# Kernel optimization log

Hardware: AMD Instinct MI355X
Metric: run time of the kernel (lower is better)

Reference implementation:

```python
import jax, jax.numpy as jnp
import numpy as np

EMBED = 1024
HEADS = 16
HEAD_DIM = EMBED // HEADS  # 64 quantum wires


def setup_inputs() -> dict:
    key = jax.random.key(0)
    ks = jax.random.split(key, 6)
    s = 1.0 / np.sqrt(EMBED)
    return {
        "x": jax.random.normal(ks[0], (8, 4096, EMBED), dtype=jnp.float32),
        "Wk": jax.random.normal(ks[1], (EMBED, EMBED), dtype=jnp.float32) * s,
        "Wq": jax.random.normal(ks[2], (EMBED, EMBED), dtype=jnp.float32) * s,
        "Wv": jax.random.normal(ks[3], (EMBED, EMBED), dtype=jnp.float32) * s,
        "Wo": jax.random.normal(ks[4], (EMBED, EMBED), dtype=jnp.float32) * s,
        "theta": jax.random.normal(ks[5], (HEAD_DIM,), dtype=jnp.float32),
    }


def reference(x, Wk, Wq, Wv, Wo, theta):
    b, s, _ = x.shape
    # linear projections (torch Linear: y = x @ W^T), split heads -> [b,s,h,d]
    def proj(W):
        return (x @ W.T).reshape(b, s, HEADS, HEAD_DIM)
    k, q, v = proj(Wk), proj(Wq), proj(Wv)
    # QLayer: per-wire RX(x_i) then trainable RX(theta_i) on |0>, measure PauliZ
    # -> <Z_i> = cos(x_i + theta_i) exactly (product state, independent wires).
    k_q = jnp.cos(k + theta)
    q_q = jnp.cos(q + theta)
    v_q = jnp.cos(v + theta)
    # Faithful to source: matmul over last two dims of [b,s,h,d] -> attention
    # across the HEADS axis ([b,s,h,h]), not across sequence.
    scores = jnp.einsum('bsid,bsjd->bsij', q_q, k_q) / jnp.sqrt(
        jnp.asarray(HEAD_DIM, dtype=x.dtype))
    attn = jax.nn.softmax(scores, axis=-1)  # dropout = identity at inference
    out = jnp.einsum('bsij,bsjd->bsid', attn, v_q).reshape(b, s, EMBED)
    return out @ Wo.T
```

## Files before the change

### kernel.cpp

```cpp
#include <hip/hip_runtime.h>
#include <hip/hip_fp16.h>

#define NTOK 32768
#define NE   1024

typedef _Float16 half_t;
typedef _Float16 f16x8 __attribute__((ext_vector_type(8)));
typedef _Float16 f16x4 __attribute__((ext_vector_type(4)));
typedef float    f32x4 __attribute__((ext_vector_type(4)));

typedef __attribute__((address_space(1))) const unsigned int guint;
typedef __attribute__((address_space(3))) unsigned int luint;

__device__ __forceinline__ void async16(const void* g, void* l) {
    __builtin_amdgcn_global_load_lds((guint*)g, (luint*)l, 16, 0, 0);
}

__global__ __launch_bounds__(256) void cvt_f32_f16(const float* __restrict__ s,
                                                   half_t* __restrict__ d, int n) {
    int i = (blockIdx.x * 256 + threadIdx.x) * 8;
    if (i >= n) return;
    float4 a = *(const float4*)(s + i);
    float4 b = *(const float4*)(s + i + 4);
    f16x8 h = {(_Float16)a.x, (_Float16)a.y, (_Float16)a.z, (_Float16)a.w,
               (_Float16)b.x, (_Float16)b.y, (_Float16)b.z, (_Float16)b.w};
    *(f16x8*)(d + i) = h;
}


#define WAITV(N) asm volatile("s_waitcnt vmcnt(" #N ")" ::: "memory")
#define BARRIER()                              \
    do {                                       \
        asm volatile("" ::: "memory");         \
        __builtin_amdgcn_s_barrier();          \
        asm volatile("" ::: "memory");         \
    } while (0)

#define ASC(b, c) (Asm + ((b) * 2 + (c)) * 8192)
#define BSC(b, c) (Bsm + ((b) * 2 + (c)) * 8192)

#define STAGE_A(dst, q, k0)                                                   \
    do {                                                                      \
        _Pragma("unroll") for (int l = 0; l < 2; ++l)                         \
            async16(Ag + (size_t)(l * 128 + (q) * 64 + rr) * K + (k0) + cc,   \
                    (char*)(dst) + l * 8192 + w * 1024);                      \
    } while (0)

#define STAGE_B(dst, r, k0)                                                   \
    do {                                                                      \
        _Pragma("unroll") for (int l = 0; l < 2; ++l)                         \
            async16(Bg + (size_t)((l * 2 + wb) * 64 + (r) * 32 + (rr & 31)) * K + \
                        (k0) + cc,                                            \
                    (char*)(dst) + l * 8192 + w * 1024);                      \
    } while (0)

#define READ_A(dstf, b, q)                                                    \
    do {                                                                      \
        _Pragma("unroll") for (int i = 0; i < 4; ++i)                         \
        _Pragma("unroll") for (int x = 0; x < 2; ++x)                         \
            dstf[i][x] = *(const f16x8*)&ASC(b, q)[(wr * 64 + i * 16 + l16) * 64 + \
                                                   (((x * 4 + quad) ^ sw) * 8)]; \
    } while (0)

#define READ_B(dstf, b, r)                                                    \
    do {                                                                      \
        _Pragma("unroll") for (int i2 = 0; i2 < 2; ++i2)                      \
        _Pragma("unroll") for (int x = 0; x < 2; ++x)                         \
            dstf[i2][x] = *(const f16x8*)&BSC(b, r)[(wc * 32 + i2 * 16 + l16) * 64 + \
                                                    (((x * 4 + quad) ^ sw) * 8)]; \
    } while (0)

#define MMA(af, bf, QA, RB)                                                   \
    do {                                                                      \
        __builtin_amdgcn_s_setprio(1);                                        \
        _Pragma("unroll") for (int i = 0; i < 4; ++i)                         \
        _Pragma("unroll") for (int jj = 0; jj < 2; ++jj)                      \
        _Pragma("unroll") for (int x = 0; x < 2; ++x)                         \
            acc[(QA) * 4 + i][(RB) * 2 + jj] =                                \
                __builtin_amdgcn_mfma_f32_16x16x32_f16(                       \
                    af[i][x], bf[jj][x], acc[(QA) * 4 + i][(RB) * 2 + jj], 0, 0, 0); \
        __builtin_amdgcn_s_setprio(0);                                        \
    } while (0)

template <bool QKV>
__global__ __launch_bounds__(512, 2) void gemm_bt(const half_t* __restrict__ A,
                                                  const half_t* __restrict__ Bbase,
                                                  void* __restrict__ Cout,
                                                  const float* __restrict__ theta) {
    constexpr int K  = 1024;
    constexpr int NT = 16;
    constexpr int J  = QKV ? 12 : 4;
    __shared__ alignas(16) half_t smem[65536];
    half_t* Asm = smem;
    half_t* Bsm = smem + 32768;

    const int id    = blockIdx.x;
    const int xcd   = id & 7;
    const int slot  = id >> 3;
    const int ygrp  = slot / J;
    const int j     = slot - ygrp * J;
    const int mtile = ygrp * 8 + xcd;
    const int zsl   = QKV ? (j >> 2) : 0;
    const int xt    = QKV ? (j & 3) : j;

    const int tid  = threadIdx.x;
    const int w    = tid >> 6;
    const int lane = tid & 63;
    const int quad = lane >> 4;
    const int l16  = lane & 15;
    const int sw   = l16 & 7;
    const int wr   = w >> 2, wc = w & 3;
    const size_t m0 = (size_t)mtile * 256;
    const int    n0 = xt * 256;

    const half_t* Ag = A + m0 * K;
    const half_t* Bg = Bbase + (size_t)zsl * (size_t)(NE * NE) + (size_t)n0 * K;

    const int rr = tid >> 3;
    const int cc = ((tid & 7) ^ (rr & 7)) * 8;
    const int wb = tid >> 8;

    f32x4 acc[8][4];
#pragma unroll
    for (int i = 0; i < 8; ++i)
#pragma unroll
        for (int jj = 0; jj < 4; ++jj) acc[i][jj] = (f32x4){0.f, 0.f, 0.f, 0.f};

    STAGE_A(ASC(0, 0), 0, 0);
    STAGE_B(BSC(0, 0), 0, 0);
    STAGE_B(BSC(0, 1), 1, 0);
    STAGE_A(ASC(0, 1), 1, 0);
    STAGE_A(ASC(1, 0), 0, 64);
    STAGE_B(BSC(1, 0), 0, 64);
    STAGE_B(BSC(1, 1), 1, 64);
    STAGE_A(ASC(1, 1), 1, 64);
    WAITV(12);
    BARRIER();

    f16x8 aF0[4][2], aF1[4][2], bF0[2][2], bF1[2][2];
    READ_A(aF0, 0, 0);
    READ_B(bF0, 0, 0);
    BARRIER();

    for (int t = 0; t < NT - 2; ++t) {
        const int cur = t & 1, nxt = cur ^ 1;
        const int kf = (t + 2) * 64;
        STAGE_A(ASC(cur, 0), 0, kf);
        MMA(aF0, bF0, 0, 0);
        WAITV(12);
        BARRIER();
        READ_B(bF1, cur, 1);
        STAGE_B(BSC(cur, 0), 0, kf);
        MMA(aF0, bF1, 0, 1);
        WAITV(12);
        BARRIER();
        READ_A(aF1, cur, 1);
        STAGE_B(BSC(cur, 1), 1, kf);
        MMA(aF1, bF1, 1, 1);
        BARRIER();
        STAGE_A(ASC(cur, 1), 1, kf);
        MMA(aF1, bF0, 1, 0);
        WAITV(12);
        BARRIER();
        READ_A(aF0, nxt, 0);
        READ_B(bF0, nxt, 0);
        BARRIER();
    }
    {
        MMA(aF0, bF0, 0, 0);
        WAITV(10);
        BARRIER();
        READ_B(bF1, 0, 1);
        MMA(aF0, bF1, 0, 1);
        WAITV(8);
        BARRIER();
        READ_A(aF1, 0, 1);
        MMA(aF1, bF1, 1, 1);
        MMA(aF1, bF0, 1, 0);
        WAITV(4);
        BARRIER();
        READ_A(aF0, 1, 0);
        READ_B(bF0, 1, 0);
    }
    {
        MMA(aF0, bF0, 0, 0);
        WAITV(2);
        BARRIER();
        READ_B(bF1, 1, 1);
        MMA(aF0, bF1, 0, 1);
        WAITV(0);
        BARRIER();
        READ_A(aF1, 1, 1);
        MMA(aF1, bF1, 1, 1);
        MMA(aF1, bF0, 1, 0);
    }
    __syncthreads();

    if (QKV) {
        half_t* Cl = smem;
#pragma unroll
        for (int nt = 0; nt < 4; ++nt) {
            const int col = wc * 64 + nt * 16 + l16;
            const float th = theta[col & 63];
#pragma unroll
            for (int mt = 0; mt < 8; ++mt) {
                const int rowb = wr * 128 + mt * 16 + quad * 4;
#pragma unroll
                for (int r = 0; r < 4; ++r) {
                    const int row = rowb + r;
                    Cl[row * 256 + (col ^ (((row >> 2) & 3) << 4))] =
                        (half_t)__cosf(acc[mt][nt][r] + th);
                }
            }
        }
        __syncthreads();
        half_t* Cg = (half_t*)Cout + (size_t)zsl * ((size_t)NTOK * NE);
#pragma unroll
        for (int it = 0; it < 16; ++it) {
            const int row = it * 16 + (tid >> 5);
            const int seg = tid & 31;
            f16x8 vv = *(const f16x8*)&Cl[row * 256 +
                                          ((seg * 8) ^ (((row >> 2) & 3) << 4))];
            *(f16x8*)&Cg[(m0 + row) * NE + n0 + seg * 8] = vv;
        }
    } else {
        float* ClF = (float*)smem;
        float* Cg  = (float*)Cout;
#pragma unroll
        for (int s = 0; s < 2; ++s) {
            if (wr == s) {
#pragma unroll
                for (int nt = 0; nt < 4; ++nt) {
                    const int col = wc * 64 + nt * 16 + l16;
#pragma unroll
                    for (int mt = 0; mt < 8; ++mt) {
                        const int rowb = mt * 16 + quad * 4;
#pragma unroll
                        for (int r = 0; r < 4; ++r) {
                            const int row = rowb + r;
                            ClF[row * 256 + (col ^ (((row >> 2) & 1) << 4))] =
                                acc[mt][nt][r];
                        }
                    }
                }
            }
            __syncthreads();
#pragma unroll
            for (int it = 0; it < 16; ++it) {
                const int row = it * 8 + (tid >> 6);
                const int seg = tid & 63;
                f32x4 vv = *(const f32x4*)&ClF[row * 256 +
                                               ((seg * 4) ^ (((row >> 2) & 1) << 4))];
                *(f32x4*)&Cg[(m0 + s * 128 + row) * NE + n0 + seg * 4] = vv;
            }
            __syncthreads();
        }
    }
}

__global__ __launch_bounds__(256) void attn_kernel(const half_t* __restrict__ q,
                                                   const half_t* __restrict__ k,
                                                   const half_t* __restrict__ v,
                                                   half_t* __restrict__ out) {
    __shared__ half_t vT[4][64][20];
    __shared__ half_t Pl[4][16][20];
    const int tid  = threadIdx.x;
    const int w    = tid >> 6;
    const int lane = tid & 63;
    const int quad = lane >> 4;
    const int l16  = lane & 15;
    const size_t base = ((size_t)blockIdx.x * 4 + w) * 1024;

    {
        const int h = lane >> 2, d0 = (lane & 3) * 16;
        f16x8 va = *(const f16x8*)(v + base + h * 64 + d0);
        f16x8 vb = *(const f16x8*)(v + base + h * 64 + d0 + 8);
#pragma unroll
        for (int z = 0; z < 8; ++z) {
            vT[w][d0 + z][h]     = va[z];
            vT[w][d0 + 8 + z][h] = vb[z];
        }
    }

    f16x8 aq0 = *(const f16x8*)(q + base + l16 * 64 + quad * 8);
    f16x8 aq1 = *(const f16x8*)(q + base + l16 * 64 + 32 + quad * 8);
    f16x8 bk0 = *(const f16x8*)(k + base + l16 * 64 + quad * 8);
    f16x8 bk1 = *(const f16x8*)(k + base + l16 * 64 + 32 + quad * 8);
    f32x4 S = __builtin_amdgcn_mfma_f32_16x16x32_f16(aq0, bk0, (f32x4){0.f,0.f,0.f,0.f}, 0, 0, 0);
    S = __builtin_amdgcn_mfma_f32_16x16x32_f16(aq1, bk1, S, 0, 0, 0);

#pragma unroll
    for (int r = 0; r < 4; ++r) {
        float s = S[r] * 0.125f;
        float mx = s;
#pragma unroll
        for (int o = 8; o; o >>= 1) mx = fmaxf(mx, __shfl_xor(mx, o));
        float e = __expf(s - mx);
        float sum = e;
#pragma unroll
        for (int o = 8; o; o >>= 1) sum += __shfl_xor(sum, o);
        Pl[w][quad * 4 + r][l16] = (half_t)(e / sum);
    }
    __syncthreads();

    f16x4 ap = *(const f16x4*)&Pl[w][l16][quad * 4];
#pragma unroll
    for (int c = 0; c < 4; ++c) {
        f16x4 bv = *(const f16x4*)&vT[w][c * 16 + l16][quad * 4];
        f32x4 O = __builtin_amdgcn_mfma_f32_16x16x16f16(ap, bv, (f32x4){0.f,0.f,0.f,0.f}, 0, 0, 0);
#pragma unroll
        for (int r = 0; r < 4; ++r)
            out[base + (quad * 4 + r) * 64 + c * 16 + l16] = (half_t)O[r];
    }
}

extern "C" void kernel_launch(void* const* d_in, const int* in_sizes, int n_in,
                              void* d_out, int out_size, void* d_ws, size_t ws_size,
                              hipStream_t stream) {
    const float* x     = (const float*)d_in[0];
    const float* Wk    = (const float*)d_in[1];
    const float* Wq    = (const float*)d_in[2];
    const float* Wv    = (const float*)d_in[3];
    const float* Wo    = (const float*)d_in[4];
    const float* theta = (const float*)d_in[5];

    char* ws = (char*)d_ws;
    half_t* xh  = (half_t*)ws;
    half_t* wh  = (half_t*)(ws + (size_t)(64 << 20));
    half_t* qkv = (half_t*)(ws + (size_t)(72 << 20));

    cvt_f32_f16<<<NTOK * NE / 2048, 256, 0, stream>>>(x, xh, NTOK * NE);
    cvt_f32_f16<<<NE * NE / 2048, 256, 0, stream>>>(Wq, wh + 0 * NE * NE, NE * NE);
    cvt_f32_f16<<<NE * NE / 2048, 256, 0, stream>>>(Wk, wh + 1 * NE * NE, NE * NE);
    cvt_f32_f16<<<NE * NE / 2048, 256, 0, stream>>>(Wv, wh + 2 * NE * NE, NE * NE);
    cvt_f32_f16<<<NE * NE / 2048, 256, 0, stream>>>(Wo, wh + 3 * NE * NE, NE * NE);

    gemm_bt<true><<<1536, 512, 0, stream>>>(xh, wh, qkv, theta);

    attn_kernel<<<NTOK / 4, 256, 0, stream>>>(qkv, qkv + (size_t)NTOK * NE,
                                              qkv + 2 * (size_t)NTOK * NE, xh);

    gemm_bt<false><<<512, 512, 0, stream>>>(xh, wh + 3 * NE * NE, d_out, nullptr);
}
```

Measured before the change: 568.7 us.

## Load GEMM B operand directly from global into registers, merge weight conversions

The GEMM no longer stages the weight (B) tiles through LDS. Each wave loads its B fragments straight from global memory into registers a k-step ahead, and only A goes through the async LDS double buffer, which cuts the number of barriers per iteration. The four weight fp32-to-fp16 conversion launches are merged into a single 2D-grid kernel. The trade-off is that B is now read uncoalesced from global/L2 with less reuse across waves, and registers carry all fragments.

```diff
diff --git a/kernel.cpp b/kernel.cpp
--- a/kernel.cpp
+++ b/kernel.cpp
@@ -27,30 +27,36 @@
     *(f16x8*)(d + i) = h;
 }
 
+__global__ __launch_bounds__(256) void cvt4_f32_f16(const float* __restrict__ s0,
+                                                    const float* __restrict__ s1,
+                                                    const float* __restrict__ s2,
+                                                    const float* __restrict__ s3,
+                                                    half_t* __restrict__ d) {
+    const float* srcs[4] = {s0, s1, s2, s3};
+    const float* s = srcs[blockIdx.y];
+    int i = (blockIdx.x * 256 + threadIdx.x) * 8;
+    float4 a = *(const float4*)(s + i);
+    float4 b = *(const float4*)(s + i + 4);
+    f16x8 h = {(_Float16)a.x, (_Float16)a.y, (_Float16)a.z, (_Float16)a.w,
+               (_Float16)b.x, (_Float16)b.y, (_Float16)b.z, (_Float16)b.w};
+    *(f16x8*)(d + (size_t)blockIdx.y * (NE * NE) + i) = h;
+}
+
 
 #define WAITV(N) asm volatile("s_waitcnt vmcnt(" #N ")" ::: "memory")
-#define BARRIER()                              \
-    do {                                       \
-        asm volatile("" ::: "memory");         \
-        __builtin_amdgcn_s_barrier();          \
-        asm volatile("" ::: "memory");         \
+#define SYNC()                                             \
+    do {                                                   \
+        asm volatile("s_waitcnt lgkmcnt(0)" ::: "memory"); \
+        __builtin_amdgcn_s_barrier();                      \
+        asm volatile("" ::: "memory");                     \
     } while (0)
 
 #define ASC(b, c) (Asm + ((b) * 2 + (c)) * 8192)
-#define BSC(b, c) (Bsm + ((b) * 2 + (c)) * 8192)
 
 #define STAGE_A(dst, q, k0)                                                   \
     do {                                                                      \
         _Pragma("unroll") for (int l = 0; l < 2; ++l)                         \
             async16(Ag + (size_t)(l * 128 + (q) * 64 + rr) * K + (k0) + cc,   \
-                    (char*)(dst) + l * 8192 + w * 1024);                      \
-    } while (0)
-
-#define STAGE_B(dst, r, k0)                                                   \
-    do {                                                                      \
-        _Pragma("unroll") for (int l = 0; l < 2; ++l)                         \
-            async16(Bg + (size_t)((l * 2 + wb) * 64 + (r) * 32 + (rr & 31)) * K + \
-                        (k0) + cc,                                            \
                     (char*)(dst) + l * 8192 + w * 1024);                      \
     } while (0)
 
@@ -62,12 +68,12 @@
                                                    (((x * 4 + quad) ^ sw) * 8)]; \
     } while (0)
 
-#define READ_B(dstf, b, r)                                                    \
+#define LOADB(dst, RB, kt)                                                    \
     do {                                                                      \
-        _Pragma("unroll") for (int i2 = 0; i2 < 2; ++i2)                      \
+        _Pragma("unroll") for (int jj = 0; jj < 2; ++jj)                      \
         _Pragma("unroll") for (int x = 0; x < 2; ++x)                         \
-            dstf[i2][x] = *(const f16x8*)&BSC(b, r)[(wc * 32 + i2 * 16 + l16) * 64 + \
-                                                    (((x * 4 + quad) ^ sw) * 8)]; \
+            dst[jj][x] = *(const f16x8*)(Bq +                                 \
+                (size_t)((RB) * 32 + jj * 16) * K + (kt) * 64 + x * 32);      \
     } while (0)
 
 #define MMA(af, bf, QA, RB)                                                   \
@@ -92,7 +98,6 @@
     constexpr int J  = QKV ? 12 : 4;
     __shared__ alignas(16) half_t smem[65536];
     half_t* Asm = smem;
-    half_t* Bsm = smem + 32768;
 
     const int id    = blockIdx.x;
     const int xcd   = id & 7;
@@ -115,10 +120,10 @@
 
     const half_t* Ag = A + m0 * K;
     const half_t* Bg = Bbase + (size_t)zsl * (size_t)(NE * NE) + (size_t)n0 * K;
+    const half_t* Bq = Bg + (size_t)(wc * 64 + l16) * K + quad * 8;
 
     const int rr = tid >> 3;
     const int cc = ((tid & 7) ^ (rr & 7)) * 8;
-    const int wb = tid >> 8;
 
     f32x4 acc[8][4];
 #pragma unroll
@@ -126,73 +131,54 @@
 #pragma unroll
         for (int jj = 0; jj < 4; ++jj) acc[i][jj] = (f32x4){0.f, 0.f, 0.f, 0.f};
 
+    f16x8 aF0[4][2], aF1[4][2], bB0[2][2], bB1[2][2];
+
     STAGE_A(ASC(0, 0), 0, 0);
-    STAGE_B(BSC(0, 0), 0, 0);
-    STAGE_B(BSC(0, 1), 1, 0);
     STAGE_A(ASC(0, 1), 1, 0);
     STAGE_A(ASC(1, 0), 0, 64);
-    STAGE_B(BSC(1, 0), 0, 64);
-    STAGE_B(BSC(1, 1), 1, 64);
+    LOADB(bB0, 0, 0);
     STAGE_A(ASC(1, 1), 1, 64);
-    WAITV(12);
-    BARRIER();
-
-    f16x8 aF0[4][2], aF1[4][2], bF0[2][2], bF1[2][2];
+    WAITV(8);
+    SYNC();
     READ_A(aF0, 0, 0);
-    READ_B(bF0, 0, 0);
-    BARRIER();
-
-    for (int t = 0; t < NT - 2; ++t) {
+    READ_A(aF1, 0, 1);
+
+    for (int t = 0; t <= NT - 3; ++t) {
         const int cur = t & 1, nxt = cur ^ 1;
         const int kf = (t + 2) * 64;
+        LOADB(bB1, 1, t);
+        MMA(aF0, bB0, 0, 0);
+        SYNC();
         STAGE_A(ASC(cur, 0), 0, kf);
-        MMA(aF0, bF0, 0, 0);
-        WAITV(12);
-        BARRIER();
-        READ_B(bF1, cur, 1);
-        STAGE_B(BSC(cur, 0), 0, kf);
-        MMA(aF0, bF1, 0, 1);
-        WAITV(12);
-        BARRIER();
-        READ_A(aF1, cur, 1);
-        STAGE_B(BSC(cur, 1), 1, kf);
-        MMA(aF1, bF1, 1, 1);
-        BARRIER();
+        MMA(aF1, bB0, 1, 0);
+        LOADB(bB0, 0, t + 1);
+        MMA(aF1, bB1, 1, 1);
+        MMA(aF0, bB1, 0, 1);
+        WAITV(10);
+        SYNC();
+        READ_A(aF0, nxt, 0);
+        READ_A(aF1, nxt, 1);
         STAGE_A(ASC(cur, 1), 1, kf);
-        MMA(aF1, bF0, 1, 0);
-        WAITV(12);
-        BARRIER();
-        READ_A(aF0, nxt, 0);
-        READ_B(bF0, nxt, 0);
-        BARRIER();
     }
     {
-        MMA(aF0, bF0, 0, 0);
-        WAITV(10);
-        BARRIER();
-        READ_B(bF1, 0, 1);
-        MMA(aF0, bF1, 0, 1);
+        LOADB(bB1, 1, NT - 2);
+        MMA(aF0, bB0, 0, 0);
+        SYNC();
+        MMA(aF1, bB0, 1, 0);
+        LOADB(bB0, 0, NT - 1);
+        MMA(aF1, bB1, 1, 1);
+        MMA(aF0, bB1, 0, 1);
         WAITV(8);
-        BARRIER();
-        READ_A(aF1, 0, 1);
-        MMA(aF1, bF1, 1, 1);
-        MMA(aF1, bF0, 1, 0);
-        WAITV(4);
-        BARRIER();
+        SYNC();
         READ_A(aF0, 1, 0);
-        READ_B(bF0, 1, 0);
+        READ_A(aF1, 1, 1);
     }
     {
-        MMA(aF0, bF0, 0, 0);
-        WAITV(2);
-        BARRIER();
-        READ_B(bF1, 1, 1);
-        MMA(aF0, bF1, 0, 1);
-        WAITV(0);
-        BARRIER();
-        READ_A(aF1, 1, 1);
-        MMA(aF1, bF1, 1, 1);
-        MMA(aF1, bF0, 1, 0);
+        LOADB(bB1, 1, NT - 1);
+        MMA(aF0, bB0, 0, 0);
+        MMA(aF1, bB0, 1, 0);
+        MMA(aF1, bB1, 1, 1);
+        MMA(aF0, bB1, 0, 1);
     }
     __syncthreads();
 
@@ -330,10 +316,7 @@
     half_t* qkv = (half_t*)(ws + (size_t)(72 << 20));
 
     cvt_f32_f16<<<NTOK * NE / 2048, 256, 0, stream>>>(x, xh, NTOK * NE);
-    cvt_f32_f16<<<NE * NE / 2048, 256, 0, stream>>>(Wq, wh + 0 * NE * NE, NE * NE);
-    cvt_f32_f16<<<NE * NE / 2048, 256, 0, stream>>>(Wk, wh + 1 * NE * NE, NE * NE);
-    cvt_f32_f16<<<NE * NE / 2048, 256, 0, stream>>>(Wv, wh + 2 * NE * NE, NE * NE);
-    cvt_f32_f16<<<NE * NE / 2048, 256, 0, stream>>>(Wo, wh + 3 * NE * NE, NE * NE);
+    cvt4_f32_f16<<<dim3(NE * NE / 2048, 4), 256, 0, stream>>>(Wq, Wk, Wv, Wo, wh);
 
     gemm_bt<true><<<1536, 512, 0, stream>>>(xh, wh, qkv, theta);
 
```

After: 675.4 us. +18.8%, slower.

## Make GEMM persistent with next-tile prefetch overlapping epilogue, merge weight conversions

Applied to the files above, without the earlier changes.

Turns the GEMM kernel into a persistent kernel with 256 blocks. Each block loops over several output tiles and prefetches the first K-slices of the next tile during the tail of the current one. The epilogue now stages its output through the free halves of the shared-memory buffers, so it no longer clobbers prefetched data. The four weight-conversion launches are merged into one 2D launch. The aim is to hide per-tile prologue and epilogue latency and cut launch overhead, at the cost of more complex wait-count bookkeeping and a possible tail imbalance with fewer blocks.

```diff
diff --git a/kernel.cpp b/kernel.cpp
--- a/kernel.cpp
+++ b/kernel.cpp
@@ -27,29 +27,50 @@
     *(f16x8*)(d + i) = h;
 }
 
+__global__ __launch_bounds__(256) void cvt4_f32_f16(const float* __restrict__ s0,
+                                                    const float* __restrict__ s1,
+                                                    const float* __restrict__ s2,
+                                                    const float* __restrict__ s3,
+                                                    half_t* __restrict__ d) {
+    const float* srcs[4] = {s0, s1, s2, s3};
+    const float* s = srcs[blockIdx.y];
+    int i = (blockIdx.x * 256 + threadIdx.x) * 8;
+    float4 a = *(const float4*)(s + i);
+    float4 b = *(const float4*)(s + i + 4);
+    f16x8 h = {(_Float16)a.x, (_Float16)a.y, (_Float16)a.z, (_Float16)a.w,
+               (_Float16)b.x, (_Float16)b.y, (_Float16)b.z, (_Float16)b.w};
+    *(f16x8*)(d + (size_t)blockIdx.y * (NE * NE) + i) = h;
+}
+
 
 #define WAITV(N) asm volatile("s_waitcnt vmcnt(" #N ")" ::: "memory")
-#define BARRIER()                              \
+#define BAR()                                  \
     do {                                       \
         asm volatile("" ::: "memory");         \
         __builtin_amdgcn_s_barrier();          \
         asm volatile("" ::: "memory");         \
     } while (0)
+#define BARL()                                             \
+    do {                                                   \
+        asm volatile("s_waitcnt lgkmcnt(0)" ::: "memory"); \
+        __builtin_amdgcn_s_barrier();                      \
+        asm volatile("" ::: "memory");                     \
+    } while (0)
 
 #define ASC(b, c) (Asm + ((b) * 2 + (c)) * 8192)
 #define BSC(b, c) (Bsm + ((b) * 2 + (c)) * 8192)
 
-#define STAGE_A(dst, q, k0)                                                   \
+#define STAGE_A(P, dst, q, k0)                                                \
     do {                                                                      \
         _Pragma("unroll") for (int l = 0; l < 2; ++l)                         \
-            async16(Ag + (size_t)(l * 128 + (q) * 64 + rr) * K + (k0) + cc,   \
+            async16((P) + (size_t)(l * 128 + (q) * 64 + rr) * K + (k0) + cc,  \
                     (char*)(dst) + l * 8192 + w * 1024);                      \
     } while (0)
 
-#define STAGE_B(dst, r, k0)                                                   \
+#define STAGE_B(P, dst, r, k0)                                                \
     do {                                                                      \
         _Pragma("unroll") for (int l = 0; l < 2; ++l)                         \
-            async16(Bg + (size_t)((l * 2 + wb) * 64 + (r) * 32 + (rr & 31)) * K + \
+            async16((P) + (size_t)((l * 2 + wb) * 64 + (r) * 32 + (rr & 31)) * K + \
                         (k0) + cc,                                            \
                     (char*)(dst) + l * 8192 + w * 1024);                      \
     } while (0)
@@ -87,21 +108,15 @@
                                                   const half_t* __restrict__ Bbase,
                                                   void* __restrict__ Cout,
                                                   const float* __restrict__ theta) {
-    constexpr int K  = 1024;
-    constexpr int NT = 16;
-    constexpr int J  = QKV ? 12 : 4;
+    constexpr int K     = 1024;
+    constexpr int J     = QKV ? 12 : 4;
+    constexpr int ITERS = QKV ? 6 : 2;
     __shared__ alignas(16) half_t smem[65536];
     half_t* Asm = smem;
     half_t* Bsm = smem + 32768;
 
-    const int id    = blockIdx.x;
-    const int xcd   = id & 7;
-    const int slot  = id >> 3;
-    const int ygrp  = slot / J;
-    const int j     = slot - ygrp * J;
-    const int mtile = ygrp * 8 + xcd;
-    const int zsl   = QKV ? (j >> 2) : 0;
-    const int xt    = QKV ? (j & 3) : j;
+    const int id  = blockIdx.x;
+    const int xcd = id & 7;
 
     const int tid  = threadIdx.x;
     const int w    = tid >> 6;
@@ -110,150 +125,210 @@
     const int l16  = lane & 15;
     const int sw   = l16 & 7;
     const int wr   = w >> 2, wc = w & 3;
-    const size_t m0 = (size_t)mtile * 256;
-    const int    n0 = xt * 256;
-
-    const half_t* Ag = A + m0 * K;
-    const half_t* Bg = Bbase + (size_t)zsl * (size_t)(NE * NE) + (size_t)n0 * K;
 
     const int rr = tid >> 3;
     const int cc = ((tid & 7) ^ (rr & 7)) * 8;
     const int wb = tid >> 8;
 
+    auto decode = [&](int v, const half_t*& Agp, const half_t*& Bgp,
+                      size_t& m0o, int& n0o, int& zso) {
+        const int slot = v >> 3;
+        const int yg   = slot / J;
+        const int jx   = slot - yg * J;
+        const int mt   = yg * 8 + xcd;
+        zso = QKV ? (jx >> 2) : 0;
+        const int xtt = QKV ? (jx & 3) : jx;
+        m0o = (size_t)mt * 256;
+        n0o = xtt * 256;
+        Agp = A + m0o * K;
+        Bgp = Bbase + (size_t)zso * (size_t)(NE * NE) + (size_t)n0o * K;
+    };
+
+    f16x8 aF0[4][2], aF1[4][2], bF0[2][2], bF1[2][2];
     f32x4 acc[8][4];
-#pragma unroll
-    for (int i = 0; i < 8; ++i)
-#pragma unroll
-        for (int jj = 0; jj < 4; ++jj) acc[i][jj] = (f32x4){0.f, 0.f, 0.f, 0.f};
-
-    STAGE_A(ASC(0, 0), 0, 0);
-    STAGE_B(BSC(0, 0), 0, 0);
-    STAGE_B(BSC(0, 1), 1, 0);
-    STAGE_A(ASC(0, 1), 1, 0);
-    STAGE_A(ASC(1, 0), 0, 64);
-    STAGE_B(BSC(1, 0), 0, 64);
-    STAGE_B(BSC(1, 1), 1, 64);
-    STAGE_A(ASC(1, 1), 1, 64);
-    WAITV(12);
-    BARRIER();
-
-    f16x8 aF0[4][2], aF1[4][2], bF0[2][2], bF1[2][2];
-    READ_A(aF0, 0, 0);
-    READ_B(bF0, 0, 0);
-    BARRIER();
-
-    for (int t = 0; t < NT - 2; ++t) {
-        const int cur = t & 1, nxt = cur ^ 1;
-        const int kf = (t + 2) * 64;
-        STAGE_A(ASC(cur, 0), 0, kf);
-        MMA(aF0, bF0, 0, 0);
-        WAITV(12);
-        BARRIER();
-        READ_B(bF1, cur, 1);
-        STAGE_B(BSC(cur, 0), 0, kf);
-        MMA(aF0, bF1, 0, 1);
-        WAITV(12);
-        BARRIER();
-        READ_A(aF1, cur, 1);
-        STAGE_B(BSC(cur, 1), 1, kf);
-        MMA(aF1, bF1, 1, 1);
-        BARRIER();
-        STAGE_A(ASC(cur, 1), 1, kf);
-        MMA(aF1, bF0, 1, 0);
-        WAITV(12);
-        BARRIER();
-        READ_A(aF0, nxt, 0);
-        READ_B(bF0, nxt, 0);
-        BARRIER();
-    }
-    {
-        MMA(aF0, bF0, 0, 0);
-        WAITV(10);
-        BARRIER();
-        READ_B(bF1, 0, 1);
-        MMA(aF0, bF1, 0, 1);
+
+    for (int it = 0; it < ITERS; ++it) {
+        const bool more = (it + 1 < ITERS);
+        const half_t *Ag, *Bg, *Agn = nullptr, *Bgn = nullptr;
+        size_t m0, m0n;
+        int n0, zsl, n0n, zn;
+        decode(id + it * 256, Ag, Bg, m0, n0, zsl);
+        if (more) decode(id + (it + 1) * 256, Agn, Bgn, m0n, n0n, zn);
+
+#pragma unroll
+        for (int i = 0; i < 8; ++i)
+#pragma unroll
+            for (int jj = 0; jj < 4; ++jj) acc[i][jj] = (f32x4){0.f, 0.f, 0.f, 0.f};
+
+        if (it == 0) {
+            STAGE_B(Bg, BSC(0, 0), 0, 0);
+            STAGE_A(Ag, ASC(0, 0), 0, 0);
+            STAGE_B(Bg, BSC(0, 1), 1, 0);
+            STAGE_A(Ag, ASC(0, 1), 1, 0);
+        }
+        STAGE_B(Bg, BSC(1, 0), 0, 64);
+        STAGE_A(Ag, ASC(1, 0), 0, 64);
+        STAGE_B(Bg, BSC(1, 1), 1, 64);
+        STAGE_A(Ag, ASC(1, 1), 1, 64);
         WAITV(8);
-        BARRIER();
-        READ_A(aF1, 0, 1);
-        MMA(aF1, bF1, 1, 1);
-        MMA(aF1, bF0, 1, 0);
-        WAITV(4);
-        BARRIER();
-        READ_A(aF0, 1, 0);
-        READ_B(bF0, 1, 0);
-    }
-    {
-        MMA(aF0, bF0, 0, 0);
-        WAITV(2);
-        BARRIER();
-        READ_B(bF1, 1, 1);
-        MMA(aF0, bF1, 0, 1);
-        WAITV(0);
-        BARRIER();
-        READ_A(aF1, 1, 1);
-        MMA(aF1, bF1, 1, 1);
-        MMA(aF1, bF0, 1, 0);
-    }
-    __syncthreads();
-
-    if (QKV) {
-        half_t* Cl = smem;
-#pragma unroll
-        for (int nt = 0; nt < 4; ++nt) {
-            const int col = wc * 64 + nt * 16 + l16;
-            const float th = theta[col & 63];
-#pragma unroll
-            for (int mt = 0; mt < 8; ++mt) {
-                const int rowb = wr * 128 + mt * 16 + quad * 4;
-#pragma unroll
-                for (int r = 0; r < 4; ++r) {
-                    const int row = rowb + r;
-                    Cl[row * 256 + (col ^ (((row >> 2) & 3) << 4))] =
-                        (half_t)__cosf(acc[mt][nt][r] + th);
-                }
-            }
+        BAR();
+        READ_A(aF0, 0, 0);
+        READ_B(bF0, 0, 0);
+        BAR();
+
+        for (int t = 0; t < 14; ++t) {
+            const int cur = t & 1, nxt = cur ^ 1;
+            const int kf = (t + 2) * 64;
+            STAGE_B(Bg, BSC(cur, 0), 0, kf);
+            MMA(aF0, bF0, 0, 0);
+            WAITV(12);
+            BAR();
+            READ_B(bF1, cur, 1);
+            STAGE_A(Ag, ASC(cur, 0), 0, kf);
+            MMA(aF0, bF1, 0, 1);
+            WAITV(12);
+            BAR();
+            READ_A(aF1, cur, 1);
+            STAGE_B(Bg, BSC(cur, 1), 1, kf);
+            MMA(aF1, bF1, 1, 1);
+            MMA(aF1, bF0, 1, 0);
+            WAITV(10);
+            BAR();
+            READ_A(aF0, nxt, 0);
+            READ_B(bF0, nxt, 0);
+            STAGE_A(Ag, ASC(cur, 1), 1, kf);
+            BAR();
         }
-        __syncthreads();
-        half_t* Cg = (half_t*)Cout + (size_t)zsl * ((size_t)NTOK * NE);
-#pragma unroll
-        for (int it = 0; it < 16; ++it) {
-            const int row = it * 16 + (tid >> 5);
-            const int seg = tid & 31;
-            f16x8 vv = *(const f16x8*)&Cl[row * 256 +
-                                          ((seg * 8) ^ (((row >> 2) & 3) << 4))];
-            *(f16x8*)&Cg[(m0 + row) * NE + n0 + seg * 8] = vv;
+        if (more) {
+            STAGE_B(Bgn, BSC(0, 0), 0, 0);
+            MMA(aF0, bF0, 0, 0);
+            WAITV(12);
+            BAR();
+            READ_B(bF1, 0, 1);
+            STAGE_A(Agn, ASC(0, 0), 0, 0);
+            MMA(aF0, bF1, 0, 1);
+            WAITV(12);
+            BAR();
+            READ_A(aF1, 0, 1);
+            STAGE_B(Bgn, BSC(0, 1), 1, 0);
+            MMA(aF1, bF1, 1, 1);
+            MMA(aF1, bF0, 1, 0);
+            WAITV(10);
+            BAR();
+            READ_A(aF0, 1, 0);
+            READ_B(bF0, 1, 0);
+            STAGE_A(Agn, ASC(0, 1), 1, 0);
+            BAR();
+            MMA(aF0, bF0, 0, 0);
+            WAITV(10);
+            BAR();
+            READ_B(bF1, 1, 1);
+            MMA(aF0, bF1, 0, 1);
+            WAITV(8);
+            BAR();
+            READ_A(aF1, 1, 1);
+            MMA(aF1, bF1, 1, 1);
+            MMA(aF1, bF0, 1, 0);
+        } else {
+            MMA(aF0, bF0, 0, 0);
+            WAITV(10);
+            BAR();
+            READ_B(bF1, 0, 1);
+            MMA(aF0, bF1, 0, 1);
+            WAITV(8);
+            BAR();
+            READ_A(aF1, 0, 1);
+            MMA(aF1, bF1, 1, 1);
+            MMA(aF1, bF0, 1, 0);
+            WAITV(4);
+            BAR();
+            READ_A(aF0, 1, 0);
+            READ_B(bF0, 1, 0);
+            MMA(aF0, bF0, 0, 0);
+            WAITV(2);
+            BAR();
+            READ_B(bF1, 1, 1);
+            MMA(aF0, bF1, 0, 1);
+            WAITV(0);
+            BAR();
+            READ_A(aF1, 1, 1);
+            MMA(aF1, bF1, 1, 1);
+            MMA(aF1, bF0, 1, 0);
         }
-    } else {
-        float* ClF = (float*)smem;
-        float* Cg  = (float*)Cout;
-#pragma unroll
-        for (int s = 0; s < 2; ++s) {
-            if (wr == s) {
-#pragma unroll
-                for (int nt = 0; nt < 4; ++nt) {
-                    const int col = wc * 64 + nt * 16 + l16;
-#pragma unroll
-                    for (int mt = 0; mt < 8; ++mt) {
-                        const int rowb = mt * 16 + quad * 4;
-#pragma unroll
-                        for (int r = 0; r < 4; ++r) {
-                            const int row = rowb + r;
-                            ClF[row * 256 + (col ^ (((row >> 2) & 1) << 4))] =
-                                acc[mt][nt][r];
+
+        BARL();
+        half_t* Ep0 = Asm + 16384;
+        half_t* Ep1 = Bsm + 16384;
+
+        if (QKV) {
+            half_t* Cg = (half_t*)Cout + (size_t)zsl * ((size_t)NTOK * NE);
+#pragma unroll
+            for (int s = 0; s < 2; ++s) {
+                if (wr == s) {
+#pragma unroll
+                    for (int nt = 0; nt < 4; ++nt) {
+                        const int col = wc * 64 + nt * 16 + l16;
+                        const float th = theta[col & 63];
+#pragma unroll
+                        for (int mt = 0; mt < 8; ++mt) {
+#pragma unroll
+                            for (int r4 = 0; r4 < 4; ++r4) {
+                                const int r = mt * 16 + quad * 4 + r4;
+                                half_t* piece = (r < 64) ? Ep0 : Ep1;
+                                piece[(r & 63) * 256 +
+                                      (col ^ (((r >> 2) & 3) << 4))] =
+                                    (half_t)__cosf(acc[mt][nt][r4] + th);
+                            }
                         }
                     }
                 }
+                BARL();
+#pragma unroll
+                for (int itx = 0; itx < 8; ++itx) {
+                    const int row = itx * 16 + (tid >> 5);
+                    const int seg = tid & 31;
+                    const half_t* piece = (row < 64) ? Ep0 : Ep1;
+                    f16x8 vv = *(const f16x8*)&piece[(row & 63) * 256 +
+                                                     ((seg * 8) ^ (((row >> 2) & 3) << 4))];
+                    *(f16x8*)&Cg[(m0 + s * 128 + row) * NE + n0 + seg * 8] = vv;
+                }
+                BARL();
             }
-            __syncthreads();
-#pragma unroll
-            for (int it = 0; it < 16; ++it) {
-                const int row = it * 8 + (tid >> 6);
-                const int seg = tid & 63;
-                f32x4 vv = *(const f32x4*)&ClF[row * 256 +
-                                               ((seg * 4) ^ (((row >> 2) & 1) << 4))];
-                *(f32x4*)&Cg[(m0 + s * 128 + row) * NE + n0 + seg * 4] = vv;
+        } else {
+            float* Cg  = (float*)Cout;
+            float* Fp0 = (float*)Ep0;
+            float* Fp1 = (float*)Ep1;
+#pragma unroll
+            for (int s = 0; s < 4; ++s) {
+                if (wr == (s >> 1)) {
+#pragma unroll
+                    for (int nt = 0; nt < 4; ++nt) {
+                        const int col = wc * 64 + nt * 16 + l16;
+#pragma unroll
+                        for (int m = 0; m < 4; ++m) {
+                            const int mt = (s & 1) * 4 + m;
+#pragma unroll
+                            for (int r4 = 0; r4 < 4; ++r4) {
+                                const int r = m * 16 + quad * 4 + r4;
+                                float* piece = (r < 32) ? Fp0 : Fp1;
+                                piece[(r & 31) * 256 +
+                                      (col ^ (((r >> 2) & 1) << 4))] = acc[mt][nt][r4];
+                            }
+                        }
+                    }
+                }
+                BARL();
+#pragma unroll
+                for (int itx = 0; itx < 8; ++itx) {
+                    const int row = itx * 8 + (tid >> 6);
+                    const int seg = tid & 63;
+                    const float* piece = (row < 32) ? Fp0 : Fp1;
+                    f32x4 vv = *(const f32x4*)&piece[(row & 31) * 256 +
+                                                     ((seg * 4) ^ (((row >> 2) & 1) << 4))];
+                    *(f32x4*)&Cg[(m0 + s * 64 + row) * NE + n0 + seg * 4] = vv;
+                }
+                BARL();
             }
-            __syncthreads();
         }
     }
 }
@@ -330,15 +405,12 @@
     half_t* qkv = (half_t*)(ws + (size_t)(72 << 20));
 
     cvt_f32_f16<<<NTOK * NE / 2048, 256, 0, stream>>>(x, xh, NTOK * NE);
-    cvt_f32_f16<<<NE * NE / 2048, 256, 0, stream>>>(Wq, wh + 0 * NE * NE, NE * NE);
-    cvt_f32_f16<<<NE * NE / 2048, 256, 0, stream>>>(Wk, wh + 1 * NE * NE, NE * NE);
-    cvt_f32_f16<<<NE * NE / 2048, 256, 0, stream>>>(Wv, wh + 2 * NE * NE, NE * NE);
-    cvt_f32_f16<<<NE * NE / 2048, 256, 0, stream>>>(Wo, wh + 3 * NE * NE, NE * NE);
-
-    gemm_bt<true><<<1536, 512, 0, stream>>>(xh, wh, qkv, theta);
+    cvt4_f32_f16<<<dim3(NE * NE / 2048, 4), 256, 0, stream>>>(Wq, Wk, Wv, Wo, wh);
+
+    gemm_bt<true><<<256, 512, 0, stream>>>(xh, wh, qkv, theta);
 
     attn_kernel<<<NTOK / 4, 256, 0, stream>>>(qkv, qkv + (size_t)NTOK * NE,
                                               qkv + 2 * (size_t)NTOK * NE, xh);
 
-    gemm_bt<false><<<512, 512, 0, stream>>>(xh, wh + 3 * NE * NE, d_out, nullptr);
-}
+    gemm_bt<false><<<256, 512, 0, stream>>>(xh, wh + 3 * NE * NE, d_out, nullptr);
+}
```

Result: slower. 1.111 ms (+95.3%).
